# Optimization experiments

Hardware: AMD Instinct MI355X
Metric: run time of the kernel (lower is better)

The kernel has to match this reference:

```python
import jax, jax.numpy as jnp
import numpy as np

BANDWITH = 10.0  # matches init kwarg `bandwith`


def setup_inputs() -> dict:
    key = jax.random.key(0)
    kx, ky = jax.random.split(key)
    X = jax.random.normal(kx, (8192, 128), dtype=jnp.float32)
    Y = jax.random.normal(ky, (8192, 128), dtype=jnp.float32)
    return {"X": X, "Y": Y}


def reference(X, Y):
    # Z = vstack([X, Y]) : [N+M, d]
    Z = jnp.concatenate([X, Y], axis=0)
    # squared euclidean cdist: ||zi||^2 + ||zj||^2 - 2 zi.zj  (clamped >= 0)
    sq = jnp.sum(Z * Z, axis=-1)  # [N+M]
    d2 = sq[:, None] + sq[None, :] - 2.0 * jnp.matmul(Z, Z.T)
    d2 = jnp.maximum(d2, 0.0)
    # RBF kernel; the original's [None,...].sum(dim=0) over a single bandwidth is identity
    K = jnp.exp(-d2 / (2.0 * BANDWITH ** 2))  # [N+M, N+M]
    n = X.shape[0]
    XX = jnp.mean(K[:n, :n])
    XY = jnp.mean(K[:n, n:])
    YY = jnp.mean(K[n:, n:])
    return XX - 2.0 * XY + YY
```

## Files before the change

### kernel.cpp

```cpp
#include <hip/hip_runtime.h>
#include <math.h>

#define TD 128
#define BT 64
#define TILE 256
#define GRIDB 512
#define NXCD 8

typedef _Float16 half8 __attribute__((ext_vector_type(8)));
typedef _Float16 half2v __attribute__((ext_vector_type(2)));
typedef float f32x4 __attribute__((ext_vector_type(4)));

#define C2f   (-0.0072134752044448f)
#define M2C2f (0.0144269504088896f)

#if __has_builtin(__builtin_amdgcn_exp2f)
#define EXP2F(x) __builtin_amdgcn_exp2f(x)
#else
#define EXP2F(x) exp2f(x)
#endif

#define LA0 0
#define LA1 16384
#define LB0 32768
#define LB1 49152
#define LEA 65536
#define LEB 66560
#define LDS_TOT 67584

#define SCHEDB() __builtin_amdgcn_sched_barrier(0)

__device__ __forceinline__ void gload16(const void* g, void* l) {
    __builtin_amdgcn_global_load_lds(
        (const __attribute__((address_space(1))) void*)g,
        (__attribute__((address_space(3))) void*)l, 16, 0, 0);
}

__device__ __forceinline__ void decode_tile(int t, int T, int& bi, int& bj) {
    double bguess = (2.0 * T + 1.0 -
                     sqrt((2.0 * T + 1.0) * (2.0 * T + 1.0) - 8.0 * (double)t)) * 0.5;
    int b = (int)bguess;
    if (b < 0) b = 0;
    if (b > T - 1) b = T - 1;
    while ((b + 1) * T - ((b + 1) * b) / 2 <= t) ++b;
    while (b * T - (b * (b - 1)) / 2 > t) --b;
    bi = b;
    bj = b + (t - (b * T - (b * (b - 1)) / 2));
}

__global__ __launch_bounds__(256) void cvt_norms_kernel(const float* __restrict__ X,
                                                        const float* __restrict__ Y,
                                                        int n, int tot,
                                                        _Float16* __restrict__ Z16,
                                                        float* __restrict__ En) {
    const int wid  = (blockIdx.x * 256 + threadIdx.x) >> 6;
    const int lane = threadIdx.x & 63;
    if (wid >= tot) return;
    const float* row = (wid < n) ? (X + (size_t)wid * TD) : (Y + (size_t)(wid - n) * TD);
    float2 v = *reinterpret_cast<const float2*>(row + lane * 2);
    _Float16 hx = (_Float16)v.x;
    _Float16 hy = (_Float16)v.y;
    half2v h2 = {hx, hy};
    *reinterpret_cast<half2v*>(Z16 + (size_t)wid * TD + lane * 2) = h2;
    float fx = (float)hx, fy = (float)hy;
    float s = fmaf(fx, fx, fy * fy);
#pragma unroll
    for (int off = 32; off > 0; off >>= 1) s += __shfl_down(s, off, 64);
    if (lane == 0) En[wid] = EXP2F(C2f * s);
}

__global__ __launch_bounds__(512, 2)
void mmd_pipe_kernel(const _Float16* __restrict__ Z16,
                     const float* __restrict__ En,
                     double* __restrict__ partials,
                     int n, int m, int T, int ntiles) {
    __shared__ char lds[LDS_TOT];

    const int tid = threadIdx.x;
    const int l = tid & 63;
    const int w = tid >> 6;
    const int lr = l & 15;
    const int kq = l >> 4;
    const int soff = (kq ^ ((lr >> 1) & 3)) << 4;
    const int wrow = (w >> 2) * 128;
    const int wcol = (w & 3) * 64;

    const int srow = tid >> 2;
    const int g16  = ((tid & 3) ^ ((tid >> 3) & 3)) << 4;
    const int ldst = w * 1024;

#define STAGE_Q(gAp, gBp, Q, LAx, LBx) do { \
        gload16((gAp) + (size_t)srow * 256 + (Q) * 64 + g16,         lds + (LAx) + ldst); \
        gload16((gAp) + (size_t)(srow + 128) * 256 + (Q) * 64 + g16, lds + (LAx) + ldst + 8192); \
        gload16((gBp) + (size_t)srow * 256 + (Q) * 64 + g16,         lds + (LBx) + ldst); \
        gload16((gBp) + (size_t)(srow + 128) * 256 + (Q) * 64 + g16, lds + (LBx) + ldst + 8192); \
    } while (0)

#define GEMM_Q(LAx, LBx, ZERO) do { \
        half8 bf[4]; \
        _Pragma("unroll") \
        for (int j = 0; j < 4; ++j) \
            bf[j] = *reinterpret_cast<const half8*>(lds + (LBx) + (wcol + j * 16 + lr) * 64 + soff); \
        __builtin_amdgcn_s_setprio(1); \
        _Pragma("unroll") \
        for (int i = 0; i < 8; ++i) { \
            half8 af = *reinterpret_cast<const half8*>(lds + (LAx) + (wrow + i * 16 + lr) * 64 + soff); \
            _Pragma("unroll") \
            for (int j = 0; j < 4; ++j) \
                acc[i][j] = __builtin_amdgcn_mfma_f32_16x16x32_f16( \
                    af, bf[j], (ZERO) ? zero4 : acc[i][j], 0, 0, 0); \
        } \
        __builtin_amdgcn_s_setprio(0); \
    } while (0)

    const f32x4 zero4 = {0.f, 0.f, 0.f, 0.f};
    double acc_d = 0.0;

    const int per_xcd = (ntiles + NXCD - 1) / NXCD;
    const int xcd = blockIdx.x & (NXCD - 1);
    const int bidx = blockIdx.x >> 3;
    const int stride = GRIDB / NXCD;
    int it = xcd * per_xcd + bidx;
    int tend = xcd * per_xcd + per_xcd;
    if (tend > ntiles) tend = ntiles;

    if (it < tend) {
        int bi, bj;
        decode_tile(it, T, bi, bj);
        const char* gA = (const char*)Z16 + (size_t)bi * (TILE * TD * 2);
        const char* gB = (const char*)Z16 + (size_t)bj * (TILE * TD * 2);

        STAGE_Q(gA, gB, 0, LA0, LB0);
        STAGE_Q(gA, gB, 1, LA1, LB1);
        if (w == 0) gload16(En + (size_t)bi * TILE + (size_t)l * 4, lds + LEA);
        if (w == 1) gload16(En + (size_t)bj * TILE + (size_t)l * 4, lds + LEB);

        while (true) {
            f32x4 acc[8][4];

            if (w < 2) asm volatile("s_waitcnt vmcnt(5)" ::: "memory");
            else       asm volatile("s_waitcnt vmcnt(4)" ::: "memory");
            SCHEDB(); __builtin_amdgcn_s_barrier(); SCHEDB();
            GEMM_Q(LA0, LB0, true);
            asm volatile("s_waitcnt lgkmcnt(0)" ::: "memory");
            __builtin_amdgcn_s_barrier(); SCHEDB();
            STAGE_Q(gA, gB, 2, LA0, LB0);

            if (w < 2) asm volatile("s_waitcnt vmcnt(5)" ::: "memory");
            else       asm volatile("s_waitcnt vmcnt(4)" ::: "memory");
            SCHEDB(); __builtin_amdgcn_s_barrier(); SCHEDB();
            GEMM_Q(LA1, LB1, false);
            asm volatile("s_waitcnt lgkmcnt(0)" ::: "memory");
            __builtin_amdgcn_s_barrier(); SCHEDB();
            STAGE_Q(gA, gB, 3, LA1, LB1);

            asm volatile("s_waitcnt vmcnt(4)" ::: "memory");
            SCHEDB(); __builtin_amdgcn_s_barrier(); SCHEDB();
            GEMM_Q(LA0, LB0, false);
            asm volatile("s_waitcnt lgkmcnt(0)" ::: "memory");
            __builtin_amdgcn_s_barrier(); SCHEDB();
            const int itn = it + stride;
            const bool more = (itn < tend);
            int bin = bi, bjn = bj;
            const char* gAn = gA;
            const char* gBn = gB;
            if (more) {
                decode_tile(itn, T, bin, bjn);
                gAn = (const char*)Z16 + (size_t)bin * (TILE * TD * 2);
                gBn = (const char*)Z16 + (size_t)bjn * (TILE * TD * 2);
                STAGE_Q(gAn, gBn, 0, LA0, LB0);
            }

            if (more) asm volatile("s_waitcnt vmcnt(4)" ::: "memory");
            else      asm volatile("s_waitcnt vmcnt(0)" ::: "memory");
            SCHEDB(); __builtin_amdgcn_s_barrier(); SCHEDB();
            GEMM_Q(LA1, LB1, false);
            asm volatile("s_waitcnt lgkmcnt(0)" ::: "memory");
            __builtin_amdgcn_s_barrier(); SCHEDB();
            if (more) STAGE_Q(gAn, gBn, 1, LA1, LB1);

            float s = 0.f;
#pragma unroll
            for (int j = 0; j < 4; ++j) {
                float Ejv = *reinterpret_cast<const float*>(lds + LEB + (wcol + j * 16 + lr) * 4);
                float sj0 = 0.f, sj1 = 0.f;
#pragma unroll
                for (int i = 0; i < 8; ++i) {
                    f32x4 Eiv = *reinterpret_cast<const f32x4*>(lds + LEA + (wrow + i * 16 + kq * 4) * 4);
#pragma unroll
                    for (int r = 0; r < 4; ++r) {
                        float e = EXP2F(M2C2f * acc[i][j][r]);
                        if (r & 1) sj1 = fmaf(Eiv[r], e, sj1);
                        else       sj0 = fmaf(Eiv[r], e, sj0);
                    }
                }
                s = fmaf(Ejv, sj0 + sj1, s);
            }

            asm volatile("s_waitcnt lgkmcnt(0)" ::: "memory");
            SCHEDB(); __builtin_amdgcn_s_barrier(); SCHEDB();
            if (more && w == 0) gload16(En + (size_t)bin * TILE + (size_t)l * 4, lds + LEA);
            if (more && w == 1) gload16(En + (size_t)bjn * TILE + (size_t)l * 4, lds + LEB);

#pragma unroll
            for (int off = 32; off > 0; off >>= 1) s += __shfl_down(s, off, 64);
            {
                double wa = (bi * TILE < n) ? (1.0 / (double)n) : (-1.0 / (double)m);
                double wb = (bj * TILE < n) ? (1.0 / (double)n) : (-1.0 / (double)m);
                double wgt = wa * wb * ((bi == bj) ? 1.0 : 2.0);
                acc_d += wgt * (double)s;
            }

            if (!more) break;
            it = itn; bi = bin; bj = bjn; gA = gAn; gB = gBn;
        }
    }

    if (l == 0) partials[(size_t)blockIdx.x * 8 + w] = acc_d;
}

__global__ __launch_bounds__(256) void norms_kernel(const float* __restrict__ X,
                                                    const float* __restrict__ Y,
                                                    int n, int tot,
                                                    float* __restrict__ norms) {
    int r = blockIdx.x * 256 + threadIdx.x;
    if (r >= tot) return;
    const float* row = (r < n) ? (X + (size_t)r * TD) : (Y + (size_t)(r - n) * TD);
    float s = 0.f;
#pragma unroll
    for (int k = 0; k < TD; k += 4) {
        float4 v = *reinterpret_cast<const float4*>(row + k);
        s = fmaf(v.x, v.x, s); s = fmaf(v.y, v.y, s);
        s = fmaf(v.z, v.z, s); s = fmaf(v.w, v.w, s);
    }
    norms[r] = s;
}

__global__ __launch_bounds__(256, 2) void mmd_tile_kernel(const float* __restrict__ X,
                                                          const float* __restrict__ Y,
                                                          const float* __restrict__ norms,
                                                          double* __restrict__ partials,
                                                          int n, int m, int T) {
    __shared__ float sA[TD][BT];
    __shared__ float sB[TD][BT];
    __shared__ float sredf[4];

    const int t = blockIdx.x;
    int bi, bj;
    decode_tile(t, T, bi, bj);

    const int tid = threadIdx.x;
    {
        const int row = tid & 63;
        const int qb  = tid >> 6;
        const int ra = bi * BT + row;
        const int rb = bj * BT + row;
        const float* Arow = (ra < n) ? (X + (size_t)ra * TD) : (Y + (size_t)(ra - n) * TD);
        const float* Brow = (rb < n) ? (X + (size_t)rb * TD) : (Y + (size_t)(rb - n) * TD);
#pragma unroll
        for (int i = 0; i < 8; ++i) {
            const int q = qb + 4 * i;
            float4 va = *reinterpret_cast<const float4*>(Arow + 4 * q);
            sA[4 * q + 0][row] = va.x; sA[4 * q + 1][row] = va.y;
            sA[4 * q + 2][row] = va.z; sA[4 * q + 3][row] = va.w;
            float4 vb = *reinterpret_cast<const float4*>(Brow + 4 * q);
            sB[4 * q + 0][row] = vb.x; sB[4 * q + 1][row] = vb.y;
            sB[4 * q + 2][row] = vb.z; sB[4 * q + 3][row] = vb.w;
        }
    }
    __syncthreads();

    const int tx = tid & 15;
    const int ty = tid >> 4;
    float acc[4][4];
#pragma unroll
    for (int i = 0; i < 4; ++i)
#pragma unroll
        for (int j = 0; j < 4; ++j) acc[i][j] = 0.f;

#pragma unroll 16
    for (int k = 0; k < TD; ++k) {
        float4 a = *reinterpret_cast<const float4*>(&sA[k][ty * 4]);
        float4 b = *reinterpret_cast<const float4*>(&sB[k][tx * 4]);
        const float av[4] = {a.x, a.y, a.z, a.w};
        const float bv[4] = {b.x, b.y, b.z, b.w};
#pragma unroll
        for (int i = 0; i < 4; ++i)
#pragma unroll
            for (int j = 0; j < 4; ++j)
                acc[i][j] = fmaf(av[i], bv[j], acc[i][j]);
    }

    float nA[4], nB[4];
#pragma unroll
    for (int i = 0; i < 4; ++i) nA[i] = norms[bi * BT + ty * 4 + i];
#pragma unroll
    for (int j = 0; j < 4; ++j) nB[j] = norms[bj * BT + tx * 4 + j];

    const float cexp = -0.005f;
    float s = 0.f;
#pragma unroll
    for (int i = 0; i < 4; ++i)
#pragma unroll
        for (int j = 0; j < 4; ++j) {
            float d2 = fmaxf(nA[i] + nB[j] - 2.f * acc[i][j], 0.f);
            s += __expf(d2 * cexp);
        }

#pragma unroll
    for (int off = 32; off > 0; off >>= 1) s += __shfl_down(s, off, 64);
    if ((tid & 63) == 0) sredf[tid >> 6] = s;
    __syncthreads();
    if (tid == 0) {
        double wa = (bi * BT < n) ? (1.0 / (double)n) : (-1.0 / (double)m);
        double wb = (bj * BT < n) ? (1.0 / (double)n) : (-1.0 / (double)m);
        double wgt = wa * wb * ((bi == bj) ? 1.0 : 2.0);
        partials[t] = wgt * (double)(sredf[0] + sredf[1] + sredf[2] + sredf[3]);
    }
}

__global__ __launch_bounds__(256) void reduce_kernel(const double* __restrict__ partials,
                                                     int npart,
                                                     float* __restrict__ out) {
    __shared__ double sd[256];
    double s = 0.0;
    for (int i = threadIdx.x; i < npart; i += 256) s += partials[i];
    sd[threadIdx.x] = s;
    __syncthreads();
    for (int off = 128; off > 0; off >>= 1) {
        if ((int)threadIdx.x < off) sd[threadIdx.x] += sd[threadIdx.x + off];
        __syncthreads();
    }
    if (threadIdx.x == 0) out[0] = (float)sd[0];
}

extern "C" void kernel_launch(void* const* d_in, const int* in_sizes, int n_in,
                              void* d_out, int out_size, void* d_ws, size_t ws_size,
                              hipStream_t stream) {
    const float* X = (const float*)d_in[0];
    const float* Y = (const float*)d_in[1];
    float* out = (float*)d_out;

    const int n = in_sizes[0] / TD;
    const int m = in_sizes[1] / TD;
    const int tot = n + m;

    const size_t z16_bytes = (size_t)tot * TD * 2;
    const size_t en_off    = (z16_bytes + 255) & ~(size_t)255;
    const size_t en_bytes  = (size_t)tot * 4;
    const size_t part_off  = ((en_off + en_bytes) + 255) & ~(size_t)255;
    const int Tm = tot / TILE;
    const int npart_m = Tm * (Tm + 1) / 2;
    const int nred = GRIDB * 8;
    const size_t needed = part_off + (size_t)nred * 8;

    if (ws_size >= needed && (tot % TILE) == 0 && (n % TILE) == 0) {
        _Float16* Z16 = (_Float16*)d_ws;
        float* En = (float*)((char*)d_ws + en_off);
        double* partials = (double*)((char*)d_ws + part_off);
        cvt_norms_kernel<<<(tot + 3) / 4, 256, 0, stream>>>(X, Y, n, tot, Z16, En);
        mmd_pipe_kernel<<<GRIDB, 512, 0, stream>>>(Z16, En, partials, n, m, Tm, npart_m);
        reduce_kernel<<<1, 256, 0, stream>>>(partials, nred, out);
    } else {
        const int T = tot / BT;
        const int npart = T * (T + 1) / 2;
        float* norms = (float*)d_ws;
        double* partials = (double*)((char*)d_ws + (((size_t)tot * 4 + 255) & ~(size_t)255));
        norms_kernel<<<(tot + 255) / 256, 256, 0, stream>>>(X, Y, n, tot, norms);
        mmd_tile_kernel<<<npart, 256, 0, stream>>>(X, Y, norms, partials, n, m, T);
        reduce_kernel<<<1, 256, 0, stream>>>(partials, npart, out);
    }
}
```

Baseline: 69.04 us.

## Replace LDS-pipelined tile GEMM with direct global-to-register MFMA loads

Drops the LDS staging buffers, async global-to-LDS loads and barrier-driven pipeline, and instead has each wave read its A and B fragments straight from global memory into registers for the MFMA loop. The block drops to 256 threads, each wave owns a 64-column slice, the tile is processed in two row halves, and the grid doubles. The exponent scale is folded into the fp16 conversion, which saves the per-element multiply before exp2. In exchange, A fragments are re-read by every wave without shared-memory reuse, which raises L2/global traffic, and without software pipelining load latency is exposed.

```diff
diff --git a/kernel.cpp b/kernel.cpp
--- a/kernel.cpp
+++ b/kernel.cpp
@@ -4,37 +4,20 @@
 #define TD 128
 #define BT 64
 #define TILE 256
-#define GRIDB 512
+#define GRIDB 1024
 #define NXCD 8
 
 typedef _Float16 half8 __attribute__((ext_vector_type(8)));
 typedef _Float16 half2v __attribute__((ext_vector_type(2)));
 typedef float f32x4 __attribute__((ext_vector_type(4)));
 
-#define C2f   (-0.0072134752044448f)
-#define M2C2f (0.0144269504088896f)
+#define SCLf 0.12011224f
 
 #if __has_builtin(__builtin_amdgcn_exp2f)
 #define EXP2F(x) __builtin_amdgcn_exp2f(x)
 #else
 #define EXP2F(x) exp2f(x)
 #endif
-
-#define LA0 0
-#define LA1 16384
-#define LB0 32768
-#define LB1 49152
-#define LEA 65536
-#define LEB 66560
-#define LDS_TOT 67584
-
-#define SCHEDB() __builtin_amdgcn_sched_barrier(0)
-
-__device__ __forceinline__ void gload16(const void* g, void* l) {
-    __builtin_amdgcn_global_load_lds(
-        (const __attribute__((address_space(1))) void*)g,
-        (__attribute__((address_space(3))) void*)l, 16, 0, 0);
-}
 
 __device__ __forceinline__ void decode_tile(int t, int T, int& bi, int& bj) {
     double bguess = (2.0 * T + 1.0 -
@@ -58,60 +41,28 @@
     if (wid >= tot) return;
     const float* row = (wid < n) ? (X + (size_t)wid * TD) : (Y + (size_t)(wid - n) * TD);
     float2 v = *reinterpret_cast<const float2*>(row + lane * 2);
-    _Float16 hx = (_Float16)v.x;
-    _Float16 hy = (_Float16)v.y;
+    _Float16 hx = (_Float16)(v.x * SCLf);
+    _Float16 hy = (_Float16)(v.y * SCLf);
     half2v h2 = {hx, hy};
     *reinterpret_cast<half2v*>(Z16 + (size_t)wid * TD + lane * 2) = h2;
     float fx = (float)hx, fy = (float)hy;
     float s = fmaf(fx, fx, fy * fy);
 #pragma unroll
     for (int off = 32; off > 0; off >>= 1) s += __shfl_down(s, off, 64);
-    if (lane == 0) En[wid] = EXP2F(C2f * s);
-}
-
-__global__ __launch_bounds__(512, 2)
-void mmd_pipe_kernel(const _Float16* __restrict__ Z16,
-                     const float* __restrict__ En,
-                     double* __restrict__ partials,
-                     int n, int m, int T, int ntiles) {
-    __shared__ char lds[LDS_TOT];
-
+    if (lane == 0) En[wid] = EXP2F(-0.5f * s);
+}
+
+__global__ __launch_bounds__(256, 2)
+void mmd_direct_kernel(const _Float16* __restrict__ Z16,
+                       const float* __restrict__ En,
+                       double* __restrict__ partials,
+                       int n, int m, int T, int ntiles) {
     const int tid = threadIdx.x;
     const int l = tid & 63;
     const int w = tid >> 6;
     const int lr = l & 15;
     const int kq = l >> 4;
-    const int soff = (kq ^ ((lr >> 1) & 3)) << 4;
-    const int wrow = (w >> 2) * 128;
-    const int wcol = (w & 3) * 64;
-
-    const int srow = tid >> 2;
-    const int g16  = ((tid & 3) ^ ((tid >> 3) & 3)) << 4;
-    const int ldst = w * 1024;
-
-#define STAGE_Q(gAp, gBp, Q, LAx, LBx) do { \
-        gload16((gAp) + (size_t)srow * 256 + (Q) * 64 + g16,         lds + (LAx) + ldst); \
-        gload16((gAp) + (size_t)(srow + 128) * 256 + (Q) * 64 + g16, lds + (LAx) + ldst + 8192); \
-        gload16((gBp) + (size_t)srow * 256 + (Q) * 64 + g16,         lds + (LBx) + ldst); \
-        gload16((gBp) + (size_t)(srow + 128) * 256 + (Q) * 64 + g16, lds + (LBx) + ldst + 8192); \
-    } while (0)
-
-#define GEMM_Q(LAx, LBx, ZERO) do { \
-        half8 bf[4]; \
-        _Pragma("unroll") \
-        for (int j = 0; j < 4; ++j) \
-            bf[j] = *reinterpret_cast<const half8*>(lds + (LBx) + (wcol + j * 16 + lr) * 64 + soff); \
-        __builtin_amdgcn_s_setprio(1); \
-        _Pragma("unroll") \
-        for (int i = 0; i < 8; ++i) { \
-            half8 af = *reinterpret_cast<const half8*>(lds + (LAx) + (wrow + i * 16 + lr) * 64 + soff); \
-            _Pragma("unroll") \
-            for (int j = 0; j < 4; ++j) \
-                acc[i][j] = __builtin_amdgcn_mfma_f32_16x16x32_f16( \
-                    af, bf[j], (ZERO) ? zero4 : acc[i][j], 0, 0, 0); \
-        } \
-        __builtin_amdgcn_s_setprio(0); \
-    } while (0)
+    const int wcol = w * 64;
 
     const f32x4 zero4 = {0.f, 0.f, 0.f, 0.f};
     double acc_d = 0.0;
@@ -120,103 +71,72 @@
     const int xcd = blockIdx.x & (NXCD - 1);
     const int bidx = blockIdx.x >> 3;
     const int stride = GRIDB / NXCD;
-    int it = xcd * per_xcd + bidx;
     int tend = xcd * per_xcd + per_xcd;
     if (tend > ntiles) tend = ntiles;
 
-    if (it < tend) {
+    for (int it = xcd * per_xcd + bidx; it < tend; it += stride) {
         int bi, bj;
         decode_tile(it, T, bi, bj);
         const char* gA = (const char*)Z16 + (size_t)bi * (TILE * TD * 2);
-        const char* gB = (const char*)Z16 + (size_t)bj * (TILE * TD * 2);
-
-        STAGE_Q(gA, gB, 0, LA0, LB0);
-        STAGE_Q(gA, gB, 1, LA1, LB1);
-        if (w == 0) gload16(En + (size_t)bi * TILE + (size_t)l * 4, lds + LEA);
-        if (w == 1) gload16(En + (size_t)bj * TILE + (size_t)l * 4, lds + LEB);
-
-        while (true) {
+        const char* gB = (const char*)Z16 + (size_t)bj * (TILE * TD * 2)
+                                          + (size_t)wcol * (TD * 2);
+        const float* EnA = En + (size_t)bi * TILE;
+        const float* EnB = En + (size_t)bj * TILE + wcol;
+
+        float s2 = 0.f;
+#pragma unroll
+        for (int half = 0; half < 2; ++half) {
+            const char* gAh = gA + half * 128 * (TD * 2);
             f32x4 acc[8][4];
 
-            if (w < 2) asm volatile("s_waitcnt vmcnt(5)" ::: "memory");
-            else       asm volatile("s_waitcnt vmcnt(4)" ::: "memory");
-            SCHEDB(); __builtin_amdgcn_s_barrier(); SCHEDB();
-            GEMM_Q(LA0, LB0, true);
-            asm volatile("s_waitcnt lgkmcnt(0)" ::: "memory");
-            __builtin_amdgcn_s_barrier(); SCHEDB();
-            STAGE_Q(gA, gB, 2, LA0, LB0);
-
-            if (w < 2) asm volatile("s_waitcnt vmcnt(5)" ::: "memory");
-            else       asm volatile("s_waitcnt vmcnt(4)" ::: "memory");
-            SCHEDB(); __builtin_amdgcn_s_barrier(); SCHEDB();
-            GEMM_Q(LA1, LB1, false);
-            asm volatile("s_waitcnt lgkmcnt(0)" ::: "memory");
-            __builtin_amdgcn_s_barrier(); SCHEDB();
-            STAGE_Q(gA, gB, 3, LA1, LB1);
-
-            asm volatile("s_waitcnt vmcnt(4)" ::: "memory");
-            SCHEDB(); __builtin_amdgcn_s_barrier(); SCHEDB();
-            GEMM_Q(LA0, LB0, false);
-            asm volatile("s_waitcnt lgkmcnt(0)" ::: "memory");
-            __builtin_amdgcn_s_barrier(); SCHEDB();
-            const int itn = it + stride;
-            const bool more = (itn < tend);
-            int bin = bi, bjn = bj;
-            const char* gAn = gA;
-            const char* gBn = gB;
-            if (more) {
-                decode_tile(itn, T, bin, bjn);
-                gAn = (const char*)Z16 + (size_t)bin * (TILE * TD * 2);
-                gBn = (const char*)Z16 + (size_t)bjn * (TILE * TD * 2);
-                STAGE_Q(gAn, gBn, 0, LA0, LB0);
+#pragma unroll
+            for (int ks = 0; ks < 4; ++ks) {
+                const int koff = ks * 64 + kq * 16;
+                half8 bf[4];
+#pragma unroll
+                for (int j = 0; j < 4; ++j)
+                    bf[j] = *reinterpret_cast<const half8*>(gB + (j * 16 + lr) * 256 + koff);
+#pragma unroll
+                for (int i = 0; i < 8; ++i) {
+                    half8 af = *reinterpret_cast<const half8*>(gAh + (i * 16 + lr) * 256 + koff);
+#pragma unroll
+                    for (int j = 0; j < 4; ++j)
+                        acc[i][j] = __builtin_amdgcn_mfma_f32_16x16x32_f16(
+                            af, bf[j], (ks == 0) ? zero4 : acc[i][j], 0, 0, 0);
+                }
             }
 
-            if (more) asm volatile("s_waitcnt vmcnt(4)" ::: "memory");
-            else      asm volatile("s_waitcnt vmcnt(0)" ::: "memory");
-            SCHEDB(); __builtin_amdgcn_s_barrier(); SCHEDB();
-            GEMM_Q(LA1, LB1, false);
-            asm volatile("s_waitcnt lgkmcnt(0)" ::: "memory");
-            __builtin_amdgcn_s_barrier(); SCHEDB();
-            if (more) STAGE_Q(gAn, gBn, 1, LA1, LB1);
-
             float s = 0.f;
 #pragma unroll
             for (int j = 0; j < 4; ++j) {
-                float Ejv = *reinterpret_cast<const float*>(lds + LEB + (wcol + j * 16 + lr) * 4);
+                float Ejv = EnB[j * 16 + lr];
                 float sj0 = 0.f, sj1 = 0.f;
 #pragma unroll
                 for (int i = 0; i < 8; ++i) {
-                    f32x4 Eiv = *reinterpret_cast<const f32x4*>(lds + LEA + (wrow + i * 16 + kq * 4) * 4);
+                    f32x4 Eiv = *reinterpret_cast<const f32x4*>(EnA + half * 128 + i * 16 + kq * 4);
 #pragma unroll
                     for (int r = 0; r < 4; ++r) {
-                        float e = EXP2F(M2C2f * acc[i][j][r]);
+                        float e = EXP2F(acc[i][j][r]);
                         if (r & 1) sj1 = fmaf(Eiv[r], e, sj1);
                         else       sj0 = fmaf(Eiv[r], e, sj0);
                     }
                 }
                 s = fmaf(Ejv, sj0 + sj1, s);
             }
-
-            asm volatile("s_waitcnt lgkmcnt(0)" ::: "memory");
-            SCHEDB(); __builtin_amdgcn_s_barrier(); SCHEDB();
-            if (more && w == 0) gload16(En + (size_t)bin * TILE + (size_t)l * 4, lds + LEA);
-            if (more && w == 1) gload16(En + (size_t)bjn * TILE + (size_t)l * 4, lds + LEB);
-
-#pragma unroll
-            for (int off = 32; off > 0; off >>= 1) s += __shfl_down(s, off, 64);
-            {
-                double wa = (bi * TILE < n) ? (1.0 / (double)n) : (-1.0 / (double)m);
-                double wb = (bj * TILE < n) ? (1.0 / (double)n) : (-1.0 / (double)m);
-                double wgt = wa * wb * ((bi == bj) ? 1.0 : 2.0);
-                acc_d += wgt * (double)s;
-            }
-
-            if (!more) break;
-            it = itn; bi = bin; bj = bjn; gA = gAn; gB = gBn;
-        }
-    }
-
-    if (l == 0) partials[(size_t)blockIdx.x * 8 + w] = acc_d;
+            s2 += s;
+        }
+
+#pragma unroll
+        for (int off = 32; off > 0; off >>= 1) s2 += __shfl_down(s2, off, 64);
+        {
+            double wa = (bi * TILE < n) ? (1.0 / (double)n) : (-1.0 / (double)m);
+            double wb = (bj * TILE < n) ? (1.0 / (double)n) : (-1.0 / (double)m);
+            double wgt = wa * wb * ((bi == bj) ? 1.0 : 2.0);
+            acc_d += wgt * (double)s2;
+        }
+    }
+
+    if (l == 0) partials[(size_t)blockIdx.x * 4 + w] = acc_d;
 }
 
 __global__ __launch_bounds__(256) void norms_kernel(const float* __restrict__ X,
@@ -351,7 +271,7 @@
     const size_t part_off  = ((en_off + en_bytes) + 255) & ~(size_t)255;
     const int Tm = tot / TILE;
     const int npart_m = Tm * (Tm + 1) / 2;
-    const int nred = GRIDB * 8;
+    const int nred = GRIDB * 4;
     const size_t needed = part_off + (size_t)nred * 8;
 
     if (ws_size >= needed && (tot % TILE) == 0 && (n % TILE) == 0) {
@@ -359,7 +279,7 @@
         float* En = (float*)((char*)d_ws + en_off);
         double* partials = (double*)((char*)d_ws + part_off);
         cvt_norms_kernel<<<(tot + 3) / 4, 256, 0, stream>>>(X, Y, n, tot, Z16, En);
-        mmd_pipe_kernel<<<GRIDB, 512, 0, stream>>>(Z16, En, partials, n, m, Tm, npart_m);
+        mmd_direct_kernel<<<GRIDB, 256, 0, stream>>>(Z16, En, partials, n, m, Tm, npart_m);
         reduce_kernel<<<1, 256, 0, stream>>>(partials, nred, out);
     } else {
         const int T = tot / BT;
```

After: 149.6 us. 117% more time.
